# Optimization experiments

Measured on AMD Instinct MI355X. Metric: run time of the kernel, lower is better.

Reference implementation:

```python
import jax, jax.numpy as jnp
import numpy as np

N_QUBITS = 8
N_CYCLES = 4
B = 8192
C64 = jnp.complex64

# ---- gate matrices ----

def _ry_batched(t):  # t: [B] -> [B,2,2]
    c = jnp.cos(t / 2).astype(C64)
    s = jnp.sin(t / 2).astype(C64)
    return jnp.stack([jnp.stack([c, -s], -1), jnp.stack([s, c], -1)], -2)


def _rz_batched(p):  # p: [B] -> [B,2,2]
    e0 = jnp.exp(-0.5j * p.astype(C64))
    e1 = jnp.exp(0.5j * p.astype(C64))
    z = jnp.zeros_like(e0)
    return jnp.stack([jnp.stack([e0, z], -1), jnp.stack([z, e1], -1)], -2)


def _rx(t):  # scalar -> [2,2]
    c = jnp.cos(t / 2).astype(C64)
    s = (-1j * jnp.sin(t / 2)).astype(C64)
    return jnp.stack([jnp.stack([c, s]), jnp.stack([s, c])])


def _crx(t):  # scalar -> [4,4] block-diag(I2, RX(t)), control = first index
    return jnp.eye(4, dtype=C64).at[2:, 2:].set(_rx(t))


def _u3(t, p, l):  # scalars -> [2,2]
    ct = jnp.cos(t / 2).astype(C64)
    st = jnp.sin(t / 2).astype(C64)
    eil = jnp.exp(1j * l.astype(C64))
    eip = jnp.exp(1j * p.astype(C64))
    return jnp.stack([jnp.stack([ct, -eil * st]), jnp.stack([eip * st, eip * eil * ct])])

CNOT = jnp.array([[1, 0, 0, 0], [0, 1, 0, 0], [0, 0, 0, 1], [0, 0, 1, 0]], dtype=C64)

# ---- statevector ops (state: [B] + [2]*N_QUBITS) ----

def apply_1q(state, U, wire):
    b = state.shape[0]
    s = jnp.moveaxis(state, 1 + wire, 1).reshape(b, 2, -1)
    s = jnp.einsum('bij,bjk->bik', U, s) if U.ndim == 3 else jnp.einsum('ij,bjk->bik', U, s)
    return jnp.moveaxis(s.reshape((b,) + (2,) * N_QUBITS), 1, 1 + wire)


def apply_2q(state, U, wc, wt):
    b = state.shape[0]
    s = jnp.moveaxis(state, (1 + wc, 1 + wt), (1, 2)).reshape(b, 4, -1)
    s = jnp.einsum('ij,bjk->bik', U, s)
    return jnp.moveaxis(s.reshape((b,) + (2,) * N_QUBITS), (1, 2), (1 + wc, 1 + wt))


def expval_z(state, wire):  # <Z_wire> : [B]
    probs = state.real ** 2 + state.imag ** 2
    axes = tuple(a for a in range(1, N_QUBITS + 1) if a != 1 + wire)
    z = jnp.sum(probs, axis=axes)  # [B,2]
    return z[:, 0] - z[:, 1]


def _circuit(theta, phi, crx_params, u3_params):
    b = theta.shape[0]
    state = jnp.zeros((b, 2 ** N_QUBITS), dtype=C64).at[:, 0].set(1.0)
    state = state.reshape((b,) + (2,) * N_QUBITS)
    # circuit builder: RY(theta), RZ(phi) on every wire + CNOT ring, n_cycles times
    U = jnp.einsum('bij,bjk->bik', _rz_batched(phi), _ry_batched(theta))  # RZ @ RY, [B,2,2]
    for _ in range(N_CYCLES):
        for w in range(N_QUBITS):
            state = apply_1q(state, U, w)
        for w in range(N_QUBITS):
            state = apply_2q(state, CNOT, w, (w + 1) % N_QUBITS)
    # QCNN layer 1
    for i, (c, t) in enumerate([(0, 1), (2, 3), (4, 5), (6, 7), (1, 2), (3, 4), (5, 6)]):
        state = apply_2q(state, _crx(crx_params[i]), c, t)
    # (intermediate expvals on [0,2,4,6] are computed then discarded in original)
    for i, w in enumerate([1, 3, 5, 7]):
        p = u3_params[i]
        state = apply_1q(state, _u3(p[0], p[1], p[2]), w)
    for i, (c, t) in enumerate([(1, 3), (5, 7), (3, 5)]):
        state = apply_2q(state, _crx(crx_params[7 + i]), c, t)
    for i, w in enumerate([3, 7]):
        p = u3_params[4 + i]
        state = apply_1q(state, _u3(p[0], p[1], p[2]), w)
    state = apply_2q(state, _crx(crx_params[10]), 3, 7)
    p = u3_params[6]
    state = apply_1q(state, _u3(p[0], p[1], p[2]), 7)
    ev = expval_z(state, 7)[:, None]  # [B,1]
    return jax.nn.relu(ev)


def setup_inputs() -> dict:
    key = jax.random.key(0)
    k1, k2, k3, k4 = jax.random.split(key, 4)
    two_pi = 2.0 * np.pi
    return {
        'theta': jax.random.uniform(k1, (B,), jnp.float32, 0.0, two_pi),
        'phi': jax.random.uniform(k2, (B,), jnp.float32, 0.0, two_pi),
        'crx_params': jax.random.uniform(k3, (11,), jnp.float32, 0.0, two_pi),
        'u3_params': jax.random.uniform(k4, (7, 3), jnp.float32, 0.0, two_pi),
    }


def reference(theta, phi, crx_params, u3_params):
    return _circuit(theta, phi, crx_params, u3_params)
```

## Files before the change

### kernel.cpp

```cpp
#include <hip/hip_runtime.h>
#include <math.h>


struct Maps { int R[8]; int V[8]; };

constexpr Maps maps_after(int ncyc) {
  Maps m{};
  for (int b = 0; b < 8; ++b) { m.R[b] = 1 << b; m.V[b] = 1 << b; }
  for (int k = 0; k < ncyc; ++k) {
    for (int w = 0; w < 8; ++w) {
      const int cb = 7 - w;
      const int tb = 7 - ((w + 1) & 7);
      m.R[tb] ^= m.R[cb];
      m.V[cb] ^= m.V[tb];
    }
  }
  return m;
}

__device__ __forceinline__ float shx(float v, int m) { return __shfl_xor(v, m, 64); }

struct G1 { float r00, i00, r01, i01, r10, i10, r11, i11; };

template <int VM, int MM>
__device__ __forceinline__ void apply_g1(float (&ar)[4], float (&ai)[4], int lane,
                                         const G1& g) {
  constexpr int vr = VM & 3, vl = VM >> 2;
  constexpr int mr = MM & 3, ml = MM >> 2;
  const bool lp = (__popc(lane & ml) & 1) != 0;
  float pr[4], pi[4];
#pragma unroll
  for (int r = 0; r < 4; ++r) {
    float xr = ar[r ^ vr], xi = ai[r ^ vr];
    if constexpr (vl != 0) { xr = shx(xr, vl); xi = shx(xi, vl); }
    pr[r] = xr; pi[r] = xi;
  }
#pragma unroll
  for (int r = 0; r < 4; ++r) {
    const bool hi = lp != ((__popc(r & mr) & 1) != 0);
    const float Ar = hi ? g.r11 : g.r00, Ai = hi ? g.i11 : g.i00;
    const float Br = hi ? g.r10 : g.r01, Bi = hi ? g.i10 : g.i01;
    const float nr = Ar * ar[r] - Ai * ai[r] + Br * pr[r] - Bi * pi[r];
    const float ni = Ar * ai[r] + Ai * ar[r] + Br * pi[r] + Bi * pr[r];
    ar[r] = nr; ai[r] = ni;
  }
}

template <int VT, int MC>
__device__ __forceinline__ void apply_crx(float (&ar)[4], float (&ai)[4], int lane,
                                          float co, float si) {
  constexpr int vr = VT & 3, vl = VT >> 2;
  constexpr int mr = MC & 3, ml = MC >> 2;
  const bool lp = (__popc(lane & ml) & 1) != 0;
  float pr[4], pi[4];
#pragma unroll
  for (int r = 0; r < 4; ++r) {
    float xr = ar[r ^ vr], xi = ai[r ^ vr];
    if constexpr (vl != 0) { xr = shx(xr, vl); xi = shx(xi, vl); }
    pr[r] = xr; pi[r] = xi;
  }
#pragma unroll
  for (int r = 0; r < 4; ++r) {
    const bool hc = lp != ((__popc(r & mr) & 1) != 0);
    const float cc = hc ? co : 1.f, ss = hc ? si : 0.f;
    const float nr = cc * ar[r] + ss * pi[r];
    const float ni = cc * ai[r] - ss * pr[r];
    ar[r] = nr; ai[r] = ni;
  }
}

__device__ __forceinline__ G1 u3_gate(const float* __restrict__ u3p, int k) {
  float st, ct, sp, cp, sl, cl;
  __sincosf(0.5f * u3p[3 * k], &st, &ct);
  __sincosf(u3p[3 * k + 1], &sp, &cp);
  __sincosf(u3p[3 * k + 2], &sl, &cl);
  G1 g;
  g.r00 = ct;        g.i00 = 0.f;
  g.r01 = -cl * st;  g.i01 = -sl * st;
  g.r10 = cp * st;   g.i10 = sp * st;
  g.r11 = (cp * cl - sp * sl) * ct;
  g.i11 = (sp * cl + cp * sl) * ct;
  return g;
}

__global__ __launch_bounds__(256, 8) void qcnn_kernel(
    const float* __restrict__ theta, const float* __restrict__ phi,
    const float* __restrict__ crx, const float* __restrict__ u3p,
    float* __restrict__ out, int nbatch) {
  const int gid = blockIdx.x * blockDim.x + threadIdx.x;
  const int b = gid >> 6;
  const int lane = threadIdx.x & 63;
  if (b >= nbatch) return;

  float ar[4], ai[4];
#pragma unroll
  for (int r = 0; r < 4; ++r) { ar[r] = 0.f; ai[r] = 0.f; }
  if (lane == 0) ar[0] = 1.f;

  const float th = theta[b], ph = phi[b];
  float sth, cth, sph, cph;
  __sincosf(0.5f * th, &sth, &cth);
  __sincosf(0.5f * ph, &sph, &cph);
  G1 U;
  U.r00 = cph * cth;  U.i00 = -sph * cth;
  U.r01 = -cph * sth; U.i01 = sph * sth;
  U.r10 = cph * sth;  U.i10 = sph * sth;
  U.r11 = cph * cth;  U.i11 = sph * cth;

  constexpr Maps M0 = maps_after(0);
  constexpr Maps M1 = maps_after(1);
  constexpr Maps M2 = maps_after(2);
  constexpr Maps M3 = maps_after(3);
  constexpr Maps MF = maps_after(4);

#define UG(M, b_) apply_g1<M.V[b_], M.R[b_]>(ar, ai, lane, U)
#define CYC(M) do { UG(M,7); UG(M,6); UG(M,5); UG(M,4); \
                    UG(M,3); UG(M,2); UG(M,1); UG(M,0); } while (0)
  CYC(M0); CYC(M1); CYC(M2); CYC(M3);
#undef CYC
#undef UG

#define CRXG(M, cb, tb, k)                                   \
  do {                                                       \
    float co_, si_;                                          \
    __sincosf(0.5f * crx[k], &si_, &co_);                    \
    apply_crx<M.V[tb], M.R[cb]>(ar, ai, lane, co_, si_);     \
  } while (0)
#define U3G(M, b_, k)                                        \
  do {                                                       \
    G1 g_ = u3_gate(u3p, k);                                 \
    apply_g1<M.V[b_], M.R[b_]>(ar, ai, lane, g_);            \
  } while (0)

  CRXG(MF, 7, 6, 0);
  CRXG(MF, 5, 4, 1);
  CRXG(MF, 3, 2, 2);
  CRXG(MF, 1, 0, 3);
  CRXG(MF, 6, 5, 4);
  CRXG(MF, 4, 3, 5);
  CRXG(MF, 2, 1, 6);

  U3G(MF, 6, 0);
  U3G(MF, 4, 1);
  U3G(MF, 2, 2);
  U3G(MF, 0, 3);

  CRXG(MF, 6, 4, 7);
  CRXG(MF, 2, 0, 8);
  CRXG(MF, 4, 2, 9);

  U3G(MF, 4, 4);
  U3G(MF, 0, 5);

  CRXG(MF, 4, 0, 10);

  U3G(MF, 0, 6);
#undef CRXG
#undef U3G

  {
    constexpr int mm = MF.R[0];
    constexpr int mr = mm & 3, ml = mm >> 2;
    const bool lp = (__popc(lane & ml) & 1) != 0;
    float v = 0.f;
#pragma unroll
    for (int r = 0; r < 4; ++r) {
      const float t = ar[r] * ar[r] + ai[r] * ai[r];
      const bool hi = lp != ((__popc(r & mr) & 1) != 0);
      v += hi ? -t : t;
    }
#pragma unroll
    for (int m = 1; m < 64; m <<= 1) v += shx(v, m);
    if (lane == 0) out[b] = fmaxf(v, 0.f);
  }
}

extern "C" void kernel_launch(void* const* d_in, const int* in_sizes, int n_in,
                              void* d_out, int out_size, void* d_ws, size_t ws_size,
                              hipStream_t stream) {
  const float* theta = (const float*)d_in[0];
  const float* phi = (const float*)d_in[1];
  const float* crx = (const float*)d_in[2];
  const float* u3p = (const float*)d_in[3];
  float* out = (float*)d_out;
  const int nb = in_sizes[0];
  const int waves_per_block = 4;
  dim3 block(64 * waves_per_block);
  dim3 grid((nb + waves_per_block - 1) / waves_per_block);
  qcnn_kernel<<<grid, block, 0, stream>>>(theta, phi, crx, u3p, out, nb);
}
```

Measured before the change: 90.58 us.

## Pack four batch states per wave with 16 amplitudes per lane

The 256-amplitude state now lives on 16 lanes with 16 register amplitudes each, where before it was spread over a full wave with 4 per lane. Each wave therefore simulates four batch elements. Gates on the register qubits need no shuffles, and the CNOT ring is done as explicit register swaps and lane shuffles instead of relabelling bits at compile time. This cuts cross-lane shuffle traffic and lets each thread do more arithmetic per shuffle. In exchange, register pressure rises sharply and launch bounds drop from 8 to 2 blocks per unit, which may lower occupancy.

```diff
diff --git a/kernel.cpp b/kernel.cpp
--- a/kernel.cpp
+++ b/kernel.cpp
@@ -2,70 +2,151 @@
 #include <math.h>
 
 
-struct Maps { int R[8]; int V[8]; };
-
-constexpr Maps maps_after(int ncyc) {
-  Maps m{};
-  for (int b = 0; b < 8; ++b) { m.R[b] = 1 << b; m.V[b] = 1 << b; }
-  for (int k = 0; k < ncyc; ++k) {
-    for (int w = 0; w < 8; ++w) {
-      const int cb = 7 - w;
-      const int tb = 7 - ((w + 1) & 7);
-      m.R[tb] ^= m.R[cb];
-      m.V[cb] ^= m.V[tb];
+__device__ __forceinline__ float shx(float v, int m) { return __shfl_xor(v, m, 64); }
+
+struct G1 { float r00, i00, r01, i01, r10, i10, r11, i11; };
+
+template <int RL, int VL>
+__device__ __forceinline__ void u_lane(float (&ar)[16], float (&ai)[16], int l,
+                                       float uAr, float uBi, float uAip,
+                                       float uAin, float uBrp, float uBrn) {
+  const bool hi = (__popc(l & RL) & 1) != 0;
+  const float Ai = hi ? uAip : uAin;
+  const float Br = hi ? uBrp : uBrn;
+  float pr[16], pi[16];
+#pragma unroll
+  for (int r = 0; r < 16; ++r) { pr[r] = shx(ar[r], VL); pi[r] = shx(ai[r], VL); }
+#pragma unroll
+  for (int r = 0; r < 16; ++r) {
+    const float nr = uAr * ar[r] - Ai * ai[r] + Br * pr[r] - uBi * pi[r];
+    const float ni = uAr * ai[r] + Ai * ar[r] + Br * pi[r] + uBi * pr[r];
+    ar[r] = nr; ai[r] = ni;
+  }
+}
+
+template <int TB>
+__device__ __forceinline__ void u_reg(float (&ar)[16], float (&ai)[16],
+                                      float uAr, float uBi, float uAip,
+                                      float uBrp) {
+#pragma unroll
+  for (int lo = 0; lo < 16; ++lo) {
+    if (lo & TB) continue;
+    const int hi = lo | TB;
+    const float lr = ar[lo], li = ai[lo], hr = ar[hi], hj = ai[hi];
+    ar[lo] = uAr * lr + uAip * li - uBrp * hr - uBi * hj;
+    ai[lo] = uAr * li - uAip * lr - uBrp * hj + uBi * hr;
+    ar[hi] = uBrp * lr - uBi * li + uAr * hr - uAip * hj;
+    ai[hi] = uBrp * li + uBi * lr + uAr * hj + uAip * hr;
+  }
+}
+
+template <int CB, int TB>
+__device__ __forceinline__ void cnot_rr(float (&ar)[16], float (&ai)[16]) {
+#pragma unroll
+  for (int r = 0; r < 16; ++r) {
+    if ((r & CB) && !(r & TB)) {
+      const int s = r | TB;
+      float t;
+      t = ar[r]; ar[r] = ar[s]; ar[s] = t;
+      t = ai[r]; ai[r] = ai[s]; ai[s] = t;
     }
   }
-  return m;
-}
-
-__device__ __forceinline__ float shx(float v, int m) { return __shfl_xor(v, m, 64); }
-
-struct G1 { float r00, i00, r01, i01, r10, i10, r11, i11; };
-
-template <int VM, int MM>
-__device__ __forceinline__ void apply_g1(float (&ar)[4], float (&ai)[4], int lane,
-                                         const G1& g) {
-  constexpr int vr = VM & 3, vl = VM >> 2;
-  constexpr int mr = MM & 3, ml = MM >> 2;
-  const bool lp = (__popc(lane & ml) & 1) != 0;
-  float pr[4], pi[4];
-#pragma unroll
-  for (int r = 0; r < 4; ++r) {
-    float xr = ar[r ^ vr], xi = ai[r ^ vr];
-    if constexpr (vl != 0) { xr = shx(xr, vl); xi = shx(xi, vl); }
-    pr[r] = xr; pi[r] = xi;
-  }
-#pragma unroll
-  for (int r = 0; r < 4; ++r) {
-    const bool hi = lp != ((__popc(r & mr) & 1) != 0);
-    const float Ar = hi ? g.r11 : g.r00, Ai = hi ? g.i11 : g.i00;
-    const float Br = hi ? g.r10 : g.r01, Bi = hi ? g.i10 : g.i01;
+}
+
+template <int RL, int TB>
+__device__ __forceinline__ void cnot_lr(float (&ar)[16], float (&ai)[16], int l) {
+  const bool c = (__popc(l & RL) & 1) != 0;
+#pragma unroll
+  for (int lo = 0; lo < 16; ++lo) {
+    if (lo & TB) continue;
+    const int hi = lo | TB;
+    float t;
+    t = c ? ar[hi] : ar[lo]; ar[hi] = c ? ar[lo] : ar[hi]; ar[lo] = t;
+    t = c ? ai[hi] : ai[lo]; ai[hi] = c ? ai[lo] : ai[hi]; ai[lo] = t;
+  }
+}
+
+template <int CB, int VL>
+__device__ __forceinline__ void cnot_rl(float (&ar)[16], float (&ai)[16]) {
+#pragma unroll
+  for (int r = 0; r < 16; ++r) {
+    if (r & CB) { ar[r] = shx(ar[r], VL); ai[r] = shx(ai[r], VL); }
+  }
+}
+
+template <int RL, int VL>
+__device__ __forceinline__ void crx_ll(float (&ar)[16], float (&ai)[16], int l,
+                                       float co, float si) {
+  const bool c = (__popc(l & RL) & 1) != 0;
+  const float cc = c ? co : 1.f, ss = c ? si : 0.f;
+  float pr[16], pi[16];
+#pragma unroll
+  for (int r = 0; r < 16; ++r) { pr[r] = shx(ar[r], VL); pi[r] = shx(ai[r], VL); }
+#pragma unroll
+  for (int r = 0; r < 16; ++r) {
+    const float nr = cc * ar[r] + ss * pi[r];
+    const float ni = cc * ai[r] - ss * pr[r];
+    ar[r] = nr; ai[r] = ni;
+  }
+}
+
+template <int CB, int TB>
+__device__ __forceinline__ void crx_rr(float (&ar)[16], float (&ai)[16],
+                                       float co, float si) {
+#pragma unroll
+  for (int lo = 0; lo < 16; ++lo) {
+    if (!(lo & CB) || (lo & TB)) continue;
+    const int hi = lo | TB;
+    const float lr = ar[lo], li = ai[lo], hr = ar[hi], hj = ai[hi];
+    ar[lo] = co * lr + si * hj;  ai[lo] = co * li - si * hr;
+    ar[hi] = co * hr + si * li;  ai[hi] = co * hj - si * lr;
+  }
+}
+
+template <int RL, int TB>
+__device__ __forceinline__ void crx_lr(float (&ar)[16], float (&ai)[16], int l,
+                                       float co, float si) {
+  const bool c = (__popc(l & RL) & 1) != 0;
+  const float cc = c ? co : 1.f, ss = c ? si : 0.f;
+#pragma unroll
+  for (int lo = 0; lo < 16; ++lo) {
+    if (lo & TB) continue;
+    const int hi = lo | TB;
+    const float lr = ar[lo], li = ai[lo], hr = ar[hi], hj = ai[hi];
+    ar[lo] = cc * lr + ss * hj;  ai[lo] = cc * li - ss * hr;
+    ar[hi] = cc * hr + ss * li;  ai[hi] = cc * hj - ss * lr;
+  }
+}
+
+template <int RL, int VL>
+__device__ __forceinline__ void u3_lane(float (&ar)[16], float (&ai)[16], int l,
+                                        const G1& g) {
+  const bool hi = (__popc(l & RL) & 1) != 0;
+  const float Ar = hi ? g.r11 : g.r00, Ai = hi ? g.i11 : g.i00;
+  const float Br = hi ? g.r10 : g.r01, Bi = hi ? g.i10 : g.i01;
+  float pr[16], pi[16];
+#pragma unroll
+  for (int r = 0; r < 16; ++r) { pr[r] = shx(ar[r], VL); pi[r] = shx(ai[r], VL); }
+#pragma unroll
+  for (int r = 0; r < 16; ++r) {
     const float nr = Ar * ar[r] - Ai * ai[r] + Br * pr[r] - Bi * pi[r];
     const float ni = Ar * ai[r] + Ai * ar[r] + Br * pi[r] + Bi * pr[r];
     ar[r] = nr; ai[r] = ni;
   }
 }
 
-template <int VT, int MC>
-__device__ __forceinline__ void apply_crx(float (&ar)[4], float (&ai)[4], int lane,
-                                          float co, float si) {
-  constexpr int vr = VT & 3, vl = VT >> 2;
-  constexpr int mr = MC & 3, ml = MC >> 2;
-  const bool lp = (__popc(lane & ml) & 1) != 0;
-  float pr[4], pi[4];
-#pragma unroll
-  for (int r = 0; r < 4; ++r) {
-    float xr = ar[r ^ vr], xi = ai[r ^ vr];
-    if constexpr (vl != 0) { xr = shx(xr, vl); xi = shx(xi, vl); }
-    pr[r] = xr; pi[r] = xi;
-  }
-#pragma unroll
-  for (int r = 0; r < 4; ++r) {
-    const bool hc = lp != ((__popc(r & mr) & 1) != 0);
-    const float cc = hc ? co : 1.f, ss = hc ? si : 0.f;
-    const float nr = cc * ar[r] + ss * pi[r];
-    const float ni = cc * ai[r] - ss * pr[r];
-    ar[r] = nr; ai[r] = ni;
+template <int TB>
+__device__ __forceinline__ void u3_reg(float (&ar)[16], float (&ai)[16],
+                                       const G1& g) {
+#pragma unroll
+  for (int lo = 0; lo < 16; ++lo) {
+    if (lo & TB) continue;
+    const int hi = lo | TB;
+    const float lr = ar[lo], li = ai[lo], hr = ar[hi], hj = ai[hi];
+    ar[lo] = g.r00 * lr - g.i00 * li + g.r01 * hr - g.i01 * hj;
+    ai[lo] = g.r00 * li + g.i00 * lr + g.r01 * hj + g.i01 * hr;
+    ar[hi] = g.r10 * lr - g.i10 * li + g.r11 * hr - g.i11 * hj;
+    ai[hi] = g.r10 * li + g.i10 * lr + g.r11 * hj + g.i11 * hr;
   }
 }
 
@@ -83,96 +164,83 @@
   return g;
 }
 
-__global__ __launch_bounds__(256, 8) void qcnn_kernel(
+__global__ __launch_bounds__(256, 2) void qcnn_kernel(
     const float* __restrict__ theta, const float* __restrict__ phi,
     const float* __restrict__ crx, const float* __restrict__ u3p,
     float* __restrict__ out, int nbatch) {
-  const int gid = blockIdx.x * blockDim.x + threadIdx.x;
-  const int b = gid >> 6;
+  const int tid = blockIdx.x * blockDim.x + threadIdx.x;
+  const int wave = tid >> 6;
   const int lane = threadIdx.x & 63;
-  if (b >= nbatch) return;
-
-  float ar[4], ai[4];
-#pragma unroll
-  for (int r = 0; r < 4; ++r) { ar[r] = 0.f; ai[r] = 0.f; }
-  if (lane == 0) ar[0] = 1.f;
+  const int l = lane & 15;
+  int b = wave * 4 + (lane >> 4);
+  if (b >= nbatch) b = nbatch - 1;
+
+  float ar[16], ai[16];
+#pragma unroll
+  for (int r = 0; r < 16; ++r) { ar[r] = 0.f; ai[r] = 0.f; }
+  if (l == 0) ar[0] = 1.f;
 
   const float th = theta[b], ph = phi[b];
   float sth, cth, sph, cph;
   __sincosf(0.5f * th, &sth, &cth);
   __sincosf(0.5f * ph, &sph, &cph);
-  G1 U;
-  U.r00 = cph * cth;  U.i00 = -sph * cth;
-  U.r01 = -cph * sth; U.i01 = sph * sth;
-  U.r10 = cph * sth;  U.i10 = sph * sth;
-  U.r11 = cph * cth;  U.i11 = sph * cth;
-
-  constexpr Maps M0 = maps_after(0);
-  constexpr Maps M1 = maps_after(1);
-  constexpr Maps M2 = maps_after(2);
-  constexpr Maps M3 = maps_after(3);
-  constexpr Maps MF = maps_after(4);
-
-#define UG(M, b_) apply_g1<M.V[b_], M.R[b_]>(ar, ai, lane, U)
-#define CYC(M) do { UG(M,7); UG(M,6); UG(M,5); UG(M,4); \
-                    UG(M,3); UG(M,2); UG(M,1); UG(M,0); } while (0)
-  CYC(M0); CYC(M1); CYC(M2); CYC(M3);
-#undef CYC
-#undef UG
-
-#define CRXG(M, cb, tb, k)                                   \
-  do {                                                       \
-    float co_, si_;                                          \
-    __sincosf(0.5f * crx[k], &si_, &co_);                    \
-    apply_crx<M.V[tb], M.R[cb]>(ar, ai, lane, co_, si_);     \
-  } while (0)
-#define U3G(M, b_, k)                                        \
-  do {                                                       \
-    G1 g_ = u3_gate(u3p, k);                                 \
-    apply_g1<M.V[b_], M.R[b_]>(ar, ai, lane, g_);            \
-  } while (0)
-
-  CRXG(MF, 7, 6, 0);
-  CRXG(MF, 5, 4, 1);
-  CRXG(MF, 3, 2, 2);
-  CRXG(MF, 1, 0, 3);
-  CRXG(MF, 6, 5, 4);
-  CRXG(MF, 4, 3, 5);
-  CRXG(MF, 2, 1, 6);
-
-  U3G(MF, 6, 0);
-  U3G(MF, 4, 1);
-  U3G(MF, 2, 2);
-  U3G(MF, 0, 3);
-
-  CRXG(MF, 6, 4, 7);
-  CRXG(MF, 2, 0, 8);
-  CRXG(MF, 4, 2, 9);
-
-  U3G(MF, 4, 4);
-  U3G(MF, 0, 5);
-
-  CRXG(MF, 4, 0, 10);
-
-  U3G(MF, 0, 6);
-#undef CRXG
-#undef U3G
-
-  {
-    constexpr int mm = MF.R[0];
-    constexpr int mr = mm & 3, ml = mm >> 2;
-    const bool lp = (__popc(lane & ml) & 1) != 0;
-    float v = 0.f;
-#pragma unroll
-    for (int r = 0; r < 4; ++r) {
-      const float t = ar[r] * ar[r] + ai[r] * ai[r];
-      const bool hi = lp != ((__popc(r & mr) & 1) != 0);
-      v += hi ? -t : t;
-    }
-#pragma unroll
-    for (int m = 1; m < 64; m <<= 1) v += shx(v, m);
-    if (lane == 0) out[b] = fmaxf(v, 0.f);
-  }
+  const float uAr = cph * cth, uBi = sph * sth;
+  const float uAip = sph * cth, uBrp = cph * sth;
+  const float uAin = -uAip, uBrn = -uBrp;
+
+#define ULANE(RL, VL) u_lane<RL, VL>(ar, ai, l, uAr, uBi, uAip, uAin, uBrp, uBrn)
+#define UREGS() do { u_reg<8>(ar, ai, uAr, uBi, uAip, uBrp); \
+                     u_reg<4>(ar, ai, uAr, uBi, uAip, uBrp); \
+                     u_reg<2>(ar, ai, uAr, uBi, uAip, uBrp); \
+                     u_reg<1>(ar, ai, uAr, uBi, uAip, uBrp); } while (0)
+#define RING(RL43, VL07) do { cnot_lr<RL43, 8>(ar, ai, l); \
+                              cnot_rr<8, 4>(ar, ai); cnot_rr<4, 2>(ar, ai); \
+                              cnot_rr<2, 1>(ar, ai); \
+                              cnot_rl<1, VL07>(ar, ai); } while (0)
+
+  ULANE(8, 8);  ULANE(4, 4);  ULANE(2, 2);  ULANE(1, 1);  UREGS(); RING(15, 12);
+  ULANE(8, 12); ULANE(12, 6); ULANE(14, 3); ULANE(15, 1); UREGS(); RING(5, 10);
+  ULANE(8, 10); ULANE(4, 5);  ULANE(10, 2); ULANE(5, 1);  UREGS(); RING(3, 15);
+  ULANE(8, 15); ULANE(12, 7); ULANE(6, 3);  ULANE(3, 1);  UREGS(); RING(1, 8);
+#undef RING
+#undef UREGS
+#undef ULANE
+
+  float co, si;
+#define LD(k) __sincosf(0.5f * crx[k], &si, &co)
+  LD(0); crx_ll<8, 4>(ar, ai, l, co, si);
+  LD(1); crx_ll<2, 1>(ar, ai, l, co, si);
+  LD(2); crx_rr<8, 4>(ar, ai, co, si);
+  LD(3); crx_rr<2, 1>(ar, ai, co, si);
+  LD(4); crx_ll<4, 2>(ar, ai, l, co, si);
+  LD(5); crx_lr<1, 8>(ar, ai, l, co, si);
+  LD(6); crx_rr<4, 2>(ar, ai, co, si);
+
+  { G1 g = u3_gate(u3p, 0); u3_lane<4, 4>(ar, ai, l, g); }
+  { G1 g = u3_gate(u3p, 1); u3_lane<1, 1>(ar, ai, l, g); }
+  { G1 g = u3_gate(u3p, 2); u3_reg<4>(ar, ai, g); }
+  { G1 g = u3_gate(u3p, 3); u3_reg<1>(ar, ai, g); }
+
+  LD(7); crx_ll<4, 1>(ar, ai, l, co, si);
+  LD(8); crx_rr<4, 1>(ar, ai, co, si);
+  LD(9); crx_lr<1, 4>(ar, ai, l, co, si);
+
+  { G1 g = u3_gate(u3p, 4); u3_lane<1, 1>(ar, ai, l, g); }
+  { G1 g = u3_gate(u3p, 5); u3_reg<1>(ar, ai, g); }
+
+  LD(10); crx_lr<1, 1>(ar, ai, l, co, si);
+
+  { G1 g = u3_gate(u3p, 6); u3_reg<1>(ar, ai, g); }
+#undef LD
+
+  float v = 0.f;
+#pragma unroll
+  for (int r = 0; r < 16; ++r) {
+    const float t = ar[r] * ar[r] + ai[r] * ai[r];
+    v += (r & 1) ? -t : t;
+  }
+  v += shx(v, 1); v += shx(v, 2); v += shx(v, 4); v += shx(v, 8);
+  if (l == 0) out[b] = fmaxf(v, 0.f);
 }
 
 extern "C" void kernel_launch(void* const* d_in, const int* in_sizes, int n_in,
@@ -184,8 +252,8 @@
   const float* u3p = (const float*)d_in[3];
   float* out = (float*)d_out;
   const int nb = in_sizes[0];
-  const int waves_per_block = 4;
-  dim3 block(64 * waves_per_block);
-  dim3 grid((nb + waves_per_block - 1) / waves_per_block);
+  const int elems_per_block = 16;
+  dim3 block(256);
+  dim3 grid((nb + elems_per_block - 1) / elems_per_block);
   qcnn_kernel<<<grid, block, 0, stream>>>(theta, phi, crx, u3p, out, nb);
 }
```

Measured after the change: 98.40 us. 8.6% more time.
